# Kernel optimization log

Hardware: AMD Instinct MI355X
Metric: run time of the kernel (lower is better)

The kernel has to match this reference:

```python
import jax, jax.numpy as jnp
import numpy as np

B, S, K, H = 2, 2048, 32, 8
IN, DM, OUT = 768, 768, 768
HD = DM // H


def setup_inputs() -> dict:
    key = jax.random.key(0)
    k0, k1, k2, k3, k4 = jax.random.split(key, 5)
    x = jax.random.normal(k0, (B, S, IN), dtype=jnp.float32)
    neighbors = jax.random.randint(k1, (B, S, K), 0, S)  # base seq indices in [0, S)
    pad = jnp.arange(S) >= int(S * 0.95)
    mask = jnp.broadcast_to(pad[None, :, None], (B, S, 1))
    # MaskedLinear to_qkv: weight (3*DM, IN), bias (3*DM); to_out: (OUT, DM), no bias
    W_qkv = jax.random.normal(k2, (3 * DM, IN), dtype=jnp.float32) * (IN ** -0.5)
    b_qkv = jax.random.normal(k3, (3 * DM,), dtype=jnp.float32) * 0.01
    W_out = jax.random.normal(k4, (OUT, DM), dtype=jnp.float32) * (DM ** -0.5)
    return {"x": x, "W_qkv": W_qkv, "b_qkv": b_qkv, "W_out": W_out,
            "neighbors": neighbors, "mask": mask}


def reference(x, W_qkv, b_qkv, W_out, neighbors, mask):
    scale = HD ** -0.5
    # to_qkv (MaskedLinear, mask_value=0.0): padded rows zeroed after projection
    qkv = x @ W_qkv.T + b_qkv                      # (B, S, 3*DM)
    qkv = jnp.where(mask, 0.0, qkv)
    q, k, v = jnp.split(qkv, 3, axis=-1)
    split_heads = lambda t: t.reshape(B, S, H, HD).transpose(0, 2, 1, 3)  # (B,H,S,HD)
    q, k, v = split_heads(q), split_heads(k), split_heads(v)

    # gather K neighbors per query (same neighbor list across heads)
    bi = jnp.arange(B)[:, None, None, None]
    hi = jnp.arange(H)[None, :, None, None]
    nb = jnp.broadcast_to(neighbors[:, None, :, :], (B, H, S, K))
    k_nb = k[bi, hi, nb]                            # (B, H, S, K, HD)
    v_nb = v[bi, hi, nb]                            # (B, H, S, K, HD)

    attn = jnp.einsum('bhnd,bhnkd->bhnk', q, k_nb) * scale  # (B, H, S, K)
    # mask gathered at neighbor positions: padded neighbors get -inf
    m_nb = mask[:, :, 0][jnp.arange(B)[:, None, None], neighbors]  # (B, S, K)
    attn = jnp.where(m_nb[:, None, :, :], -jnp.inf, attn)
    w = jax.nn.softmax(attn, axis=-1)               # dropout = 0.0

    out = jnp.einsum('bhnk,bhnkd->bhnd', w, v_nb)   # (B, H, S, HD)
    out = out.transpose(0, 2, 1, 3).reshape(B, S, DM)
    # to_out (MaskedLinear, bias=False, mask_value=0.0)
    out = out @ W_out.T
    out = jnp.where(mask, 0.0, out)
    return out
```

## Files before the change

kernel.cpp:

```cpp
#include <hip/hip_runtime.h>
#include <hip/hip_bf16.h>
#include <math.h>


#define S_LEN 2048
#define NPAD 1945
#define DMODEL 768
#define LDAB 1536

typedef __attribute__((ext_vector_type(4))) float f32x4;
typedef __attribute__((ext_vector_type(8))) _Float16 f16x8;
typedef __attribute__((ext_vector_type(4))) _Float16 f16x4;

static __device__ __forceinline__ void async16(const void* g, void* l) {
  __builtin_amdgcn_global_load_lds(
      (const __attribute__((address_space(1))) unsigned int*)g,
      (__attribute__((address_space(3))) unsigned int*)l, 16, 0, 0);
}

__global__ __launch_bounds__(256) void cast3_kernel(
    const float* __restrict__ x, const float* __restrict__ wq,
    const float* __restrict__ wo,
    _Float16* __restrict__ Ah, _Float16* __restrict__ Bq,
    _Float16* __restrict__ Bo)
{
  int i = blockIdx.x * 256 + threadIdx.x;
  const float* s; _Float16* d; int off;
  if (i < 786432)       { s = x;  d = Ah; off = i; }
  else if (i < 1228800) { s = wq; d = Bq; off = i - 786432; }
  else if (i < 1376256) { s = wo; d = Bo; off = i - 1228800; }
  else return;
  float4 v = ((const float4*)s)[off];
  f16x4 o = {(_Float16)v.x, (_Float16)v.y, (_Float16)v.z, (_Float16)v.w};
  ((f16x4*)d)[off] = o;
}

template<int BN, bool QKV>
__global__ __launch_bounds__(256, 2) void gemm_f16(
    const _Float16* __restrict__ A,
    const _Float16* __restrict__ B,
    const float* __restrict__ bias,
    float* __restrict__ C,
    _Float16* __restrict__ Kh, _Float16* __restrict__ Vh,
    int N)
{
  constexpr int NF = BN / 32;
  constexpr int NISS = (128 + BN) / 64;
  __shared__ _Float16 As[2][128 * 32];
  __shared__ _Float16 Bs[2][BN * 32];
  const int t = threadIdx.x;
  const int lane = t & 63;
  const int wave = t >> 6;
  const int wr = wave >> 1, wc = wave & 1;
  const int lr = lane & 15, lg = lane >> 4;

  const int nwg_x = gridDim.x;
  const int nwg = nwg_x * gridDim.y;
  int bid = blockIdx.y * nwg_x + blockIdx.x;
  bid = (bid & 7) * (nwg >> 3) + (bid >> 3);
  const int brow = (bid % nwg_x) * 128;
  const int bcol = (bid / nwg_x) * BN;

  const char* gA = (const char*)A + (size_t)brow * LDAB;
  const char* gB = (const char*)B + (size_t)bcol * LDAB;

  auto stage = [&](int bb, int kt) {
    const int kb = kt * 64;
#pragma unroll
    for (int i = 0; i < NISS; ++i) {
      const int off = i * 4096 + t * 16;
      if (off < 8192) {
        async16(gA + (size_t)(off >> 6) * LDAB + kb + (off & 63),
                (char*)As[bb] + off);
      } else {
        const int oo = off - 8192;
        async16(gB + (size_t)(oo >> 6) * LDAB + kb + (oo & 63),
                (char*)Bs[bb] + oo);
      }
    }
  };

  f32x4 acc[4][NF];
#pragma unroll
  for (int i = 0; i < 4; ++i)
#pragma unroll
    for (int j = 0; j < NF; ++j) acc[i][j] = (f32x4)0.f;

  stage(0, 0);
  __syncthreads();

  int cur = 0;
  for (int kt = 0; kt < 24; ++kt) {
    if (kt + 1 < 24) stage(cur ^ 1, kt + 1);

    f16x8 af[4], bf[NF];
#pragma unroll
    for (int m = 0; m < 4; ++m)
      af[m] = *(const f16x8*)((const char*)As[cur] + (wr * 64 + m * 16 + lr) * 64 + lg * 16);
#pragma unroll
    for (int n = 0; n < NF; ++n)
      bf[n] = *(const f16x8*)((const char*)Bs[cur] + (wc * (BN / 2) + n * 16 + lr) * 64 + lg * 16);
#pragma unroll
    for (int m = 0; m < 4; ++m)
#pragma unroll
      for (int n = 0; n < NF; ++n)
        acc[m][n] = __builtin_amdgcn_mfma_f32_16x16x32_f16(af[m], bf[n],
                                                           acc[m][n], 0, 0, 0);
    __syncthreads();
    cur ^= 1;
  }

#pragma unroll
  for (int m = 0; m < 4; ++m) {
    const int row0 = brow + wr * 64 + m * 16 + lg * 4;
#pragma unroll
    for (int n = 0; n < NF; ++n) {
      const int col = bcol + wc * (BN / 2) + n * 16 + lr;
      const float bs = bias ? bias[col] : 0.f;
      f32x4 v = acc[m][n];
#pragma unroll
      for (int r = 0; r < 4; ++r) {
        const int rg = row0 + r;
        const int s = rg & (S_LEN - 1);
        const float val = (s >= NPAD) ? 0.f : (v[r] + bs);
        if (QKV) {
          if (col < DMODEL) {
            C[(size_t)rg * DMODEL + col] = val;
          } else if (col < 2 * DMODEL) {
            const int e = col - DMODEL;
            const int ch = e >> 3, o = e & 7;
            const int h = ch / 12, k = ch % 12;
            Kh[(size_t)rg * DMODEL + ((h + 8 * k) << 3) + o] = (_Float16)val;
          } else {
            Vh[(size_t)rg * DMODEL + (col - 2 * DMODEL)] = (_Float16)val;
          }
        } else {
          C[(size_t)rg * N + col] = val;
        }
      }
    }
  }
}

#define NPRE 12
__global__ __launch_bounds__(256) void attn_kernel(
    const float* __restrict__ Qf,
    const _Float16* __restrict__ Kh,
    const _Float16* __restrict__ Vh,
    const int* __restrict__ neighbors,
    _Float16* __restrict__ Ao)
{
  const int bid = blockIdx.x;
  const int xcd = bid & 7, slot = bid >> 3;
  const int bch = xcd >> 2;
  const int s   = slot * 4 + (xcd & 3);
  const int m   = bch * S_LEN + s;
  const int t   = threadIdx.x;

  _Float16* orow = Ao + (size_t)m * DMODEL;
  if (s >= NPAD) {
    if (t < 192) ((f16x4*)orow)[t] = (f16x4)(_Float16)0.f;
    return;
  }

  __shared__ float qs2[8 * 100];
  __shared__ float scf[288];
  __shared__ float ws[256];
  __shared__ int nb[32];

  if (t < 32) nb[t] = neighbors[(size_t)m * 32 + t];
  if (t < 192) {
    float4 v = ((const float4*)(Qf + (size_t)m * DMODEL))[t];
    const int h = t / 24, wi = t * 4 - h * 96;
    *(float4*)(qs2 + h * 100 + wi) = v;
  }
  __syncthreads();

  f16x4 vpre[NPRE];
  if (t < 192) {
#pragma unroll
    for (int jj = 0; jj < NPRE; ++jj)
      vpre[jj] = *(const f16x4*)(Vh + (size_t)(bch * S_LEN + nb[jj]) * DMODEL + t * 4);
  }

  {
    const int lane = t & 63, w = t >> 6;
    const int r = lane >> 3, h = lane & 7;
    const int j = w * 8 + r;
    const _Float16* kbase = Kh + (size_t)(bch * S_LEN + nb[j]) * DMODEL;
    f16x8 kv[12];
#pragma unroll
    for (int k = 0; k < 12; ++k)
      kv[k] = *(const f16x8*)(kbase + ((h + 8 * k) << 3));
    float sc = 0.f;
#pragma unroll
    for (int k = 0; k < 12; ++k) {
      const float4 qa = *(const float4*)(qs2 + h * 100 + k * 8);
      const float4 qb = *(const float4*)(qs2 + h * 100 + k * 8 + 4);
      sc += (float)kv[k][0] * qa.x + (float)kv[k][1] * qa.y +
            (float)kv[k][2] * qa.z + (float)kv[k][3] * qa.w +
            (float)kv[k][4] * qb.x + (float)kv[k][5] * qb.y +
            (float)kv[k][6] * qb.z + (float)kv[k][7] * qb.w;
    }
    scf[j * 9 + h] = sc * 0.10206207261596575f;
  }
  __syncthreads();

  {
    const int h = t >> 5, j = t & 31;
    const bool masked = (nb[j] >= NPAD);
    const float sc = scf[j * 9 + h];
    float mx = masked ? -1e30f : sc;
#pragma unroll
    for (int off = 16; off >= 1; off >>= 1) mx = fmaxf(mx, __shfl_xor(mx, off));
    float p = masked ? 0.f : expf(sc - mx);
    float sum = p;
#pragma unroll
    for (int off = 16; off >= 1; off >>= 1) sum += __shfl_xor(sum, off);
    ws[t] = p / sum;
  }
  __syncthreads();

  if (t < 192) {
    const int d0 = t * 4;
    const int hh = t / 24;
    const float* wsh = ws + hh * 32;
    f32x4 acc = (f32x4)0.f;
#pragma unroll
    for (int jj = 0; jj < NPRE; ++jj) {
      const float w = wsh[jj];
      acc[0] += w * (float)vpre[jj][0];
      acc[1] += w * (float)vpre[jj][1];
      acc[2] += w * (float)vpre[jj][2];
      acc[3] += w * (float)vpre[jj][3];
    }
#pragma unroll 8
    for (int jj = NPRE; jj < 32; ++jj) {
      const f16x4 v = *(const f16x4*)(Vh + (size_t)(bch * S_LEN + nb[jj]) * DMODEL + d0);
      const float w = wsh[jj];
      acc[0] += w * (float)v[0];
      acc[1] += w * (float)v[1];
      acc[2] += w * (float)v[2];
      acc[3] += w * (float)v[3];
    }
    f16x4 o = {(_Float16)acc[0], (_Float16)acc[1], (_Float16)acc[2], (_Float16)acc[3]};
    ((f16x4*)orow)[t] = o;
  }
}

extern "C" void kernel_launch(void* const* d_in, const int* in_sizes, int n_in,
                              void* d_out, int out_size, void* d_ws, size_t ws_size,
                              hipStream_t stream) {
  const float* x       = (const float*)d_in[0];
  const float* W_qkv   = (const float*)d_in[1];
  const float* b_qkv   = (const float*)d_in[2];
  const float* W_out   = (const float*)d_in[3];
  const int*   nbr     = (const int*)d_in[4];
  float* out = (float*)d_out;

  char* ws = (char*)d_ws;
  _Float16* Ah = (_Float16*)(ws);
  _Float16* Bq = (_Float16*)(ws +  6291456);
  _Float16* Bo = (_Float16*)(ws +  9830400);
  float*    Qf = (float*)   (ws + 11010048);
  _Float16* Kh = (_Float16*)(ws + 23592960);
  _Float16* Vh = (_Float16*)(ws + 29884416);
  _Float16* Ao = Ah;

  cast3_kernel<<<5376, 256, 0, stream>>>(x, W_qkv, W_out, Ah, Bq, Bo);

  gemm_f16<128, true><<<dim3(32, 18), 256, 0, stream>>>(Ah, Bq, b_qkv,
                                                        Qf, Kh, Vh, 3 * DMODEL);
  attn_kernel<<<4096, 256, 0, stream>>>(Qf, Kh, Vh, nbr, Ao);
  gemm_f16<64, false><<<dim3(32, 12), 256, 0, stream>>>(Ao, Bo, nullptr,
                                                        out, nullptr, nullptr, DMODEL);
}
```

Before: 156.1 us.

## Halve GEMM M-tile and process two query rows per attention block

The GEMMs now take a template BM and use 64-row tiles with launch bounds of 4 waves per SIMD, which doubles the grid so more workgroups fill the CUs. The attention kernel handles two consecutive queries per block, interleaving their K and V gathers to raise memory-level parallelism and halving the block count. It also drops the V prefetch into registers. Risks are more tile overhead and B reloads in the GEMMs, plus higher register pressure and a branch in the attention inner loop.

```diff
diff --git a/kernel.cpp b/kernel.cpp
--- a/kernel.cpp
+++ b/kernel.cpp
@@ -35,8 +35,8 @@
   ((f16x4*)d)[off] = o;
 }
 
-template<int BN, bool QKV>
-__global__ __launch_bounds__(256, 2) void gemm_f16(
+template<int BM, int BN, bool QKV>
+__global__ __launch_bounds__(256, 4) void gemm_f16(
     const _Float16* __restrict__ A,
     const _Float16* __restrict__ B,
     const float* __restrict__ bias,
@@ -44,9 +44,11 @@
     _Float16* __restrict__ Kh, _Float16* __restrict__ Vh,
     int N)
 {
+  constexpr int MF = BM / 32;
   constexpr int NF = BN / 32;
-  constexpr int NISS = (128 + BN) / 64;
-  __shared__ _Float16 As[2][128 * 32];
+  constexpr int ABYTES = BM * 64;
+  constexpr int NISS = (BM + BN) / 64;
+  __shared__ _Float16 As[2][BM * 32];
   __shared__ _Float16 Bs[2][BN * 32];
   const int t = threadIdx.x;
   const int lane = t & 63;
@@ -58,7 +60,7 @@
   const int nwg = nwg_x * gridDim.y;
   int bid = blockIdx.y * nwg_x + blockIdx.x;
   bid = (bid & 7) * (nwg >> 3) + (bid >> 3);
-  const int brow = (bid % nwg_x) * 128;
+  const int brow = (bid % nwg_x) * BM;
   const int bcol = (bid / nwg_x) * BN;
 
   const char* gA = (const char*)A + (size_t)brow * LDAB;
@@ -69,20 +71,20 @@
 #pragma unroll
     for (int i = 0; i < NISS; ++i) {
       const int off = i * 4096 + t * 16;
-      if (off < 8192) {
+      if (off < ABYTES) {
         async16(gA + (size_t)(off >> 6) * LDAB + kb + (off & 63),
                 (char*)As[bb] + off);
       } else {
-        const int oo = off - 8192;
+        const int oo = off - ABYTES;
         async16(gB + (size_t)(oo >> 6) * LDAB + kb + (oo & 63),
                 (char*)Bs[bb] + oo);
       }
     }
   };
 
-  f32x4 acc[4][NF];
-#pragma unroll
-  for (int i = 0; i < 4; ++i)
+  f32x4 acc[MF][NF];
+#pragma unroll
+  for (int i = 0; i < MF; ++i)
 #pragma unroll
     for (int j = 0; j < NF; ++j) acc[i][j] = (f32x4)0.f;
 
@@ -93,15 +95,15 @@
   for (int kt = 0; kt < 24; ++kt) {
     if (kt + 1 < 24) stage(cur ^ 1, kt + 1);
 
-    f16x8 af[4], bf[NF];
-#pragma unroll
-    for (int m = 0; m < 4; ++m)
-      af[m] = *(const f16x8*)((const char*)As[cur] + (wr * 64 + m * 16 + lr) * 64 + lg * 16);
+    f16x8 af[MF], bf[NF];
+#pragma unroll
+    for (int m = 0; m < MF; ++m)
+      af[m] = *(const f16x8*)((const char*)As[cur] + (wr * (BM / 2) + m * 16 + lr) * 64 + lg * 16);
 #pragma unroll
     for (int n = 0; n < NF; ++n)
       bf[n] = *(const f16x8*)((const char*)Bs[cur] + (wc * (BN / 2) + n * 16 + lr) * 64 + lg * 16);
 #pragma unroll
-    for (int m = 0; m < 4; ++m)
+    for (int m = 0; m < MF; ++m)
 #pragma unroll
       for (int n = 0; n < NF; ++n)
         acc[m][n] = __builtin_amdgcn_mfma_f32_16x16x32_f16(af[m], bf[n],
@@ -111,8 +113,8 @@
   }
 
 #pragma unroll
-  for (int m = 0; m < 4; ++m) {
-    const int row0 = brow + wr * 64 + m * 16 + lg * 4;
+  for (int m = 0; m < MF; ++m) {
+    const int row0 = brow + wr * (BM / 2) + m * 16 + lg * 4;
 #pragma unroll
     for (int n = 0; n < NF; ++n) {
       const int col = bcol + wc * (BN / 2) + n * 16 + lr;
@@ -142,7 +144,6 @@
   }
 }
 
-#define NPRE 12
 __global__ __launch_bounds__(256) void attn_kernel(
     const float* __restrict__ Qf,
     const _Float16* __restrict__ Kh,
@@ -153,98 +154,132 @@
   const int bid = blockIdx.x;
   const int xcd = bid & 7, slot = bid >> 3;
   const int bch = xcd >> 2;
-  const int s   = slot * 4 + (xcd & 3);
-  const int m   = bch * S_LEN + s;
+  const int u   = slot * 4 + (xcd & 3);
+  const int s0  = u * 2, s1 = s0 + 1;
+  const int m0  = bch * S_LEN + s0, m1 = m0 + 1;
   const int t   = threadIdx.x;
 
-  _Float16* orow = Ao + (size_t)m * DMODEL;
-  if (s >= NPAD) {
-    if (t < 192) ((f16x4*)orow)[t] = (f16x4)(_Float16)0.f;
+  _Float16* orow0 = Ao + (size_t)m0 * DMODEL;
+  _Float16* orow1 = Ao + (size_t)m1 * DMODEL;
+  const bool act0 = (s0 < NPAD), act1 = (s1 < NPAD);
+  if (!act0) {
+    if (t < 192) {
+      ((f16x4*)orow0)[t] = (f16x4)(_Float16)0.f;
+      ((f16x4*)orow1)[t] = (f16x4)(_Float16)0.f;
+    }
     return;
   }
 
-  __shared__ float qs2[8 * 100];
-  __shared__ float scf[288];
-  __shared__ float ws[256];
-  __shared__ int nb[32];
-
-  if (t < 32) nb[t] = neighbors[(size_t)m * 32 + t];
-  if (t < 192) {
-    float4 v = ((const float4*)(Qf + (size_t)m * DMODEL))[t];
-    const int h = t / 24, wi = t * 4 - h * 96;
-    *(float4*)(qs2 + h * 100 + wi) = v;
+  __shared__ float qs2[2][800];
+  __shared__ float scf[2][288];
+  __shared__ float ws[2][256];
+  __shared__ int nb[2][32];
+
+  if (t < 64) nb[t >> 5][t & 31] = neighbors[(size_t)m0 * 32 + t];
+  {
+    if (t < 192) {
+      float4 v = ((const float4*)(Qf + (size_t)m0 * DMODEL))[t];
+      const int h = t / 24, wi = t * 4 - h * 96;
+      *(float4*)(qs2[0] + h * 100 + wi) = v;
+    }
+    if (t >= 64) {
+      const int i = t - 64;
+      float4 v = ((const float4*)(Qf + (size_t)m1 * DMODEL))[i];
+      const int h = i / 24, wi = i * 4 - h * 96;
+      *(float4*)(qs2[1] + h * 100 + wi) = v;
+    }
   }
   __syncthreads();
-
-  f16x4 vpre[NPRE];
-  if (t < 192) {
-#pragma unroll
-    for (int jj = 0; jj < NPRE; ++jj)
-      vpre[jj] = *(const f16x4*)(Vh + (size_t)(bch * S_LEN + nb[jj]) * DMODEL + t * 4);
-  }
 
   {
     const int lane = t & 63, w = t >> 6;
-    const int r = lane >> 3, h = lane & 7;
-    const int j = w * 8 + r;
-    const _Float16* kbase = Kh + (size_t)(bch * S_LEN + nb[j]) * DMODEL;
-    f16x8 kv[12];
-#pragma unroll
-    for (int k = 0; k < 12; ++k)
-      kv[k] = *(const f16x8*)(kbase + ((h + 8 * k) << 3));
-    float sc = 0.f;
+    const int nbw = lane >> 3, h = lane & 7;
+    const int j = w * 8 + nbw;
+    const _Float16* kb0 = Kh + (size_t)(bch * S_LEN + nb[0][j]) * DMODEL;
+    const _Float16* kb1 = Kh + (size_t)(bch * S_LEN + nb[1][j]) * DMODEL;
+    float sc0 = 0.f, sc1 = 0.f;
 #pragma unroll
     for (int k = 0; k < 12; ++k) {
-      const float4 qa = *(const float4*)(qs2 + h * 100 + k * 8);
-      const float4 qb = *(const float4*)(qs2 + h * 100 + k * 8 + 4);
-      sc += (float)kv[k][0] * qa.x + (float)kv[k][1] * qa.y +
-            (float)kv[k][2] * qa.z + (float)kv[k][3] * qa.w +
-            (float)kv[k][4] * qb.x + (float)kv[k][5] * qb.y +
-            (float)kv[k][6] * qb.z + (float)kv[k][7] * qb.w;
-    }
-    scf[j * 9 + h] = sc * 0.10206207261596575f;
+      const f16x8 k0 = *(const f16x8*)(kb0 + ((h + 8 * k) << 3));
+      const f16x8 k1 = *(const f16x8*)(kb1 + ((h + 8 * k) << 3));
+      const float4 qa0 = *(const float4*)(qs2[0] + h * 100 + k * 8);
+      const float4 qb0 = *(const float4*)(qs2[0] + h * 100 + k * 8 + 4);
+      const float4 qa1 = *(const float4*)(qs2[1] + h * 100 + k * 8);
+      const float4 qb1 = *(const float4*)(qs2[1] + h * 100 + k * 8 + 4);
+      sc0 += (float)k0[0] * qa0.x + (float)k0[1] * qa0.y +
+             (float)k0[2] * qa0.z + (float)k0[3] * qa0.w +
+             (float)k0[4] * qb0.x + (float)k0[5] * qb0.y +
+             (float)k0[6] * qb0.z + (float)k0[7] * qb0.w;
+      sc1 += (float)k1[0] * qa1.x + (float)k1[1] * qa1.y +
+             (float)k1[2] * qa1.z + (float)k1[3] * qa1.w +
+             (float)k1[4] * qb1.x + (float)k1[5] * qb1.y +
+             (float)k1[6] * qb1.z + (float)k1[7] * qb1.w;
+    }
+    scf[0][j * 9 + h] = sc0 * 0.10206207261596575f;
+    scf[1][j * 9 + h] = sc1 * 0.10206207261596575f;
   }
   __syncthreads();
 
   {
     const int h = t >> 5, j = t & 31;
-    const bool masked = (nb[j] >= NPAD);
-    const float sc = scf[j * 9 + h];
-    float mx = masked ? -1e30f : sc;
-#pragma unroll
-    for (int off = 16; off >= 1; off >>= 1) mx = fmaxf(mx, __shfl_xor(mx, off));
-    float p = masked ? 0.f : expf(sc - mx);
-    float sum = p;
-#pragma unroll
-    for (int off = 16; off >= 1; off >>= 1) sum += __shfl_xor(sum, off);
-    ws[t] = p / sum;
+    {
+      const bool masked = (nb[0][j] >= NPAD);
+      const float sc = scf[0][j * 9 + h];
+      float mx = masked ? -1e30f : sc;
+#pragma unroll
+      for (int off = 16; off >= 1; off >>= 1) mx = fmaxf(mx, __shfl_xor(mx, off));
+      float p = masked ? 0.f : expf(sc - mx);
+      float sum = p;
+#pragma unroll
+      for (int off = 16; off >= 1; off >>= 1) sum += __shfl_xor(sum, off);
+      ws[0][t] = p / sum;
+    }
+    if (act1) {
+      const bool masked = (nb[1][j] >= NPAD);
+      const float sc = scf[1][j * 9 + h];
+      float mx = masked ? -1e30f : sc;
+#pragma unroll
+      for (int off = 16; off >= 1; off >>= 1) mx = fmaxf(mx, __shfl_xor(mx, off));
+      float p = masked ? 0.f : expf(sc - mx);
+      float sum = p;
+#pragma unroll
+      for (int off = 16; off >= 1; off >>= 1) sum += __shfl_xor(sum, off);
+      ws[1][t] = p / sum;
+    }
   }
   __syncthreads();
 
   if (t < 192) {
     const int d0 = t * 4;
     const int hh = t / 24;
-    const float* wsh = ws + hh * 32;
-    f32x4 acc = (f32x4)0.f;
-#pragma unroll
-    for (int jj = 0; jj < NPRE; ++jj) {
-      const float w = wsh[jj];
-      acc[0] += w * (float)vpre[jj][0];
-      acc[1] += w * (float)vpre[jj][1];
-      acc[2] += w * (float)vpre[jj][2];
-      acc[3] += w * (float)vpre[jj][3];
-    }
+    const float* wsh0 = ws[0] + hh * 32;
+    const float* wsh1 = ws[1] + hh * 32;
+    f32x4 acc0 = (f32x4)0.f, acc1 = (f32x4)0.f;
 #pragma unroll 8
-    for (int jj = NPRE; jj < 32; ++jj) {
-      const f16x4 v = *(const f16x4*)(Vh + (size_t)(bch * S_LEN + nb[jj]) * DMODEL + d0);
-      const float w = wsh[jj];
-      acc[0] += w * (float)v[0];
-      acc[1] += w * (float)v[1];
-      acc[2] += w * (float)v[2];
-      acc[3] += w * (float)v[3];
-    }
-    f16x4 o = {(_Float16)acc[0], (_Float16)acc[1], (_Float16)acc[2], (_Float16)acc[3]};
-    ((f16x4*)orow)[t] = o;
+    for (int jj = 0; jj < 32; ++jj) {
+      const f16x4 v0 = *(const f16x4*)(Vh + (size_t)(bch * S_LEN + nb[0][jj]) * DMODEL + d0);
+      const float w0 = wsh0[jj];
+      acc0[0] += w0 * (float)v0[0];
+      acc0[1] += w0 * (float)v0[1];
+      acc0[2] += w0 * (float)v0[2];
+      acc0[3] += w0 * (float)v0[3];
+      if (act1) {
+        const f16x4 v1 = *(const f16x4*)(Vh + (size_t)(bch * S_LEN + nb[1][jj]) * DMODEL + d0);
+        const float w1 = wsh1[jj];
+        acc1[0] += w1 * (float)v1[0];
+        acc1[1] += w1 * (float)v1[1];
+        acc1[2] += w1 * (float)v1[2];
+        acc1[3] += w1 * (float)v1[3];
+      }
+    }
+    f16x4 o0 = {(_Float16)acc0[0], (_Float16)acc0[1], (_Float16)acc0[2], (_Float16)acc0[3]};
+    ((f16x4*)orow0)[t] = o0;
+    if (act1) {
+      f16x4 o1 = {(_Float16)acc1[0], (_Float16)acc1[1], (_Float16)acc1[2], (_Float16)acc1[3]};
+      ((f16x4*)orow1)[t] = o1;
+    } else {
+      ((f16x4*)orow1)[t] = (f16x4)(_Float16)0.f;
+    }
   }
 }
 
@@ -269,9 +304,9 @@
 
   cast3_kernel<<<5376, 256, 0, stream>>>(x, W_qkv, W_out, Ah, Bq, Bo);
 
-  gemm_f16<128, true><<<dim3(32, 18), 256, 0, stream>>>(Ah, Bq, b_qkv,
-                                                        Qf, Kh, Vh, 3 * DMODEL);
-  attn_kernel<<<4096, 256, 0, stream>>>(Qf, Kh, Vh, nbr, Ao);
-  gemm_f16<64, false><<<dim3(32, 12), 256, 0, stream>>>(Ao, Bo, nullptr,
-                                                        out, nullptr, nullptr, DMODEL);
-}
+  gemm_f16<64, 128, true><<<dim3(64, 18), 256, 0, stream>>>(Ah, Bq, b_qkv,
+                                                            Qf, Kh, Vh, 3 * DMODEL);
+  attn_kernel<<<2048, 256, 0, stream>>>(Qf, Kh, Vh, nbr, Ao);
+  gemm_f16<64, 64, false><<<dim3(64, 12), 256, 0, stream>>>(Ao, Bo, nullptr,
+                                                            out, nullptr, nullptr, DMODEL);
+}
```

Result: no change. 155.7 us (-0.3%).

## Split attention blocks by head-half over two queries and shrink GEMM M tiles

Applied to the files above, without the earlier changes.

The attention kernel now has each block handle two consecutive query rows for half of the heads (four heads, 384 dims), instead of one row for all eight heads. It also drops the V prefetch registers and loads K fragments inside the dot-product loop. Both GEMMs move from 128-row to 64-row tiles with twice as many workgroups and a launch bound of 4 blocks per SM, to fill more CUs. The cost is less data reuse per GEMM tile and possibly more exposed gather latency in attention, since the prefetch is gone.

```diff
diff --git a/kernel.cpp b/kernel.cpp
--- a/kernel.cpp
+++ b/kernel.cpp
@@ -35,8 +35,8 @@
   ((f16x4*)d)[off] = o;
 }
 
-template<int BN, bool QKV>
-__global__ __launch_bounds__(256, 2) void gemm_f16(
+template<int BM, int BN, bool QKV>
+__global__ __launch_bounds__(256, 4) void gemm_f16(
     const _Float16* __restrict__ A,
     const _Float16* __restrict__ B,
     const float* __restrict__ bias,
@@ -44,9 +44,11 @@
     _Float16* __restrict__ Kh, _Float16* __restrict__ Vh,
     int N)
 {
+  constexpr int MF = BM / 32;
   constexpr int NF = BN / 32;
-  constexpr int NISS = (128 + BN) / 64;
-  __shared__ _Float16 As[2][128 * 32];
+  constexpr int ABYTES = BM * 64;
+  constexpr int NISS = (BM + BN) / 64;
+  __shared__ _Float16 As[2][BM * 32];
   __shared__ _Float16 Bs[2][BN * 32];
   const int t = threadIdx.x;
   const int lane = t & 63;
@@ -58,7 +60,7 @@
   const int nwg = nwg_x * gridDim.y;
   int bid = blockIdx.y * nwg_x + blockIdx.x;
   bid = (bid & 7) * (nwg >> 3) + (bid >> 3);
-  const int brow = (bid % nwg_x) * 128;
+  const int brow = (bid % nwg_x) * BM;
   const int bcol = (bid / nwg_x) * BN;
 
   const char* gA = (const char*)A + (size_t)brow * LDAB;
@@ -69,20 +71,20 @@
 #pragma unroll
     for (int i = 0; i < NISS; ++i) {
       const int off = i * 4096 + t * 16;
-      if (off < 8192) {
+      if (off < ABYTES) {
         async16(gA + (size_t)(off >> 6) * LDAB + kb + (off & 63),
                 (char*)As[bb] + off);
       } else {
-        const int oo = off - 8192;
+        const int oo = off - ABYTES;
         async16(gB + (size_t)(oo >> 6) * LDAB + kb + (oo & 63),
                 (char*)Bs[bb] + oo);
       }
     }
   };
 
-  f32x4 acc[4][NF];
-#pragma unroll
-  for (int i = 0; i < 4; ++i)
+  f32x4 acc[MF][NF];
+#pragma unroll
+  for (int i = 0; i < MF; ++i)
 #pragma unroll
     for (int j = 0; j < NF; ++j) acc[i][j] = (f32x4)0.f;
 
@@ -93,15 +95,15 @@
   for (int kt = 0; kt < 24; ++kt) {
     if (kt + 1 < 24) stage(cur ^ 1, kt + 1);
 
-    f16x8 af[4], bf[NF];
-#pragma unroll
-    for (int m = 0; m < 4; ++m)
-      af[m] = *(const f16x8*)((const char*)As[cur] + (wr * 64 + m * 16 + lr) * 64 + lg * 16);
+    f16x8 af[MF], bf[NF];
+#pragma unroll
+    for (int m = 0; m < MF; ++m)
+      af[m] = *(const f16x8*)((const char*)As[cur] + (wr * (BM / 2) + m * 16 + lr) * 64 + lg * 16);
 #pragma unroll
     for (int n = 0; n < NF; ++n)
       bf[n] = *(const f16x8*)((const char*)Bs[cur] + (wc * (BN / 2) + n * 16 + lr) * 64 + lg * 16);
 #pragma unroll
-    for (int m = 0; m < 4; ++m)
+    for (int m = 0; m < MF; ++m)
 #pragma unroll
       for (int n = 0; n < NF; ++n)
         acc[m][n] = __builtin_amdgcn_mfma_f32_16x16x32_f16(af[m], bf[n],
@@ -111,8 +113,8 @@
   }
 
 #pragma unroll
-  for (int m = 0; m < 4; ++m) {
-    const int row0 = brow + wr * 64 + m * 16 + lg * 4;
+  for (int m = 0; m < MF; ++m) {
+    const int row0 = brow + wr * (BM / 2) + m * 16 + lg * 4;
 #pragma unroll
     for (int n = 0; n < NF; ++n) {
       const int col = bcol + wc * (BN / 2) + n * 16 + lr;
@@ -142,7 +144,6 @@
   }
 }
 
-#define NPRE 12
 __global__ __launch_bounds__(256) void attn_kernel(
     const float* __restrict__ Qf,
     const _Float16* __restrict__ Kh,
@@ -152,99 +153,97 @@
 {
   const int bid = blockIdx.x;
   const int xcd = bid & 7, slot = bid >> 3;
-  const int bch = xcd >> 2;
-  const int s   = slot * 4 + (xcd & 3);
-  const int m   = bch * S_LEN + s;
+  const int p   = xcd >> 1;
+  const int bch = p >> 1;
+  const int dh  = p & 1;
+  const int u   = slot * 2 + (xcd & 1);
+  const int s0  = u * 2, s1 = s0 + 1;
+  const int m0  = bch * S_LEN + s0, m1 = m0 + 1;
+  const int hbase = dh * 4, dbase = dh * 384;
   const int t   = threadIdx.x;
 
-  _Float16* orow = Ao + (size_t)m * DMODEL;
-  if (s >= NPAD) {
-    if (t < 192) ((f16x4*)orow)[t] = (f16x4)(_Float16)0.f;
+  _Float16* o0 = Ao + (size_t)m0 * DMODEL + dbase;
+  _Float16* o1 = Ao + (size_t)m1 * DMODEL + dbase;
+  const bool act1 = (s1 < NPAD);
+  if (s0 >= NPAD) {
+    if (t < 192) {
+      const int row = t / 96, i = t - row * 96;
+      ((f16x4*)(row ? o1 : o0))[i] = (f16x4)(_Float16)0.f;
+    }
     return;
   }
 
-  __shared__ float qs2[8 * 100];
-  __shared__ float scf[288];
-  __shared__ float ws[256];
-  __shared__ int nb[32];
-
-  if (t < 32) nb[t] = neighbors[(size_t)m * 32 + t];
+  __shared__ float qs[2][400];
+  __shared__ float scf[2][300];
+  __shared__ float ws[2][128];
+  __shared__ int nb[2][32];
+
+  if (t < 64) nb[t >> 5][t & 31] = neighbors[(size_t)m0 * 32 + t];
   if (t < 192) {
-    float4 v = ((const float4*)(Qf + (size_t)m * DMODEL))[t];
-    const int h = t / 24, wi = t * 4 - h * 96;
-    *(float4*)(qs2 + h * 100 + wi) = v;
-  }
-  __syncthreads();
-
-  f16x4 vpre[NPRE];
+    const int row = t / 96, i = t - row * 96;
+    float4 v = ((const float4*)(Qf + (size_t)(row ? m1 : m0) * DMODEL + dbase))[i];
+    const int h = i / 24, wi = (i - h * 24) * 4;
+    *(float4*)(qs[row] + h * 100 + wi) = v;
+  }
+  __syncthreads();
+
+  {
+    const int row = t >> 7, rem = t & 127;
+    const int h = rem & 3, j = rem >> 2;
+    const _Float16* kb = Kh + (size_t)(bch * S_LEN + nb[row][j]) * DMODEL;
+    float sc = 0.f;
+#pragma unroll
+    for (int k = 0; k < 12; ++k) {
+      const f16x8 kv = *(const f16x8*)(kb + ((hbase + h + 8 * k) << 3));
+      const float4 qa = *(const float4*)(qs[row] + h * 100 + k * 8);
+      const float4 qb = *(const float4*)(qs[row] + h * 100 + k * 8 + 4);
+      sc += (float)kv[0] * qa.x + (float)kv[1] * qa.y +
+            (float)kv[2] * qa.z + (float)kv[3] * qa.w +
+            (float)kv[4] * qb.x + (float)kv[5] * qb.y +
+            (float)kv[6] * qb.z + (float)kv[7] * qb.w;
+    }
+    scf[row][j * 9 + h] = sc * 0.10206207261596575f;
+  }
+  __syncthreads();
+
+  {
+    const int row = t >> 7, h = (t >> 5) & 3, j = t & 31;
+    const bool masked = (nb[row][j] >= NPAD);
+    const float sc = scf[row][j * 9 + h];
+    float mx = masked ? -1e30f : sc;
+#pragma unroll
+    for (int off = 16; off >= 1; off >>= 1) mx = fmaxf(mx, __shfl_xor(mx, off));
+    float pp = masked ? 0.f : expf(sc - mx);
+    float sum = pp;
+#pragma unroll
+    for (int off = 16; off >= 1; off >>= 1) sum += __shfl_xor(sum, off);
+    ws[row][h * 32 + j] = pp / sum;
+  }
+  __syncthreads();
+
   if (t < 192) {
-#pragma unroll
-    for (int jj = 0; jj < NPRE; ++jj)
-      vpre[jj] = *(const f16x4*)(Vh + (size_t)(bch * S_LEN + nb[jj]) * DMODEL + t * 4);
-  }
-
-  {
-    const int lane = t & 63, w = t >> 6;
-    const int r = lane >> 3, h = lane & 7;
-    const int j = w * 8 + r;
-    const _Float16* kbase = Kh + (size_t)(bch * S_LEN + nb[j]) * DMODEL;
-    f16x8 kv[12];
-#pragma unroll
-    for (int k = 0; k < 12; ++k)
-      kv[k] = *(const f16x8*)(kbase + ((h + 8 * k) << 3));
-    float sc = 0.f;
-#pragma unroll
-    for (int k = 0; k < 12; ++k) {
-      const float4 qa = *(const float4*)(qs2 + h * 100 + k * 8);
-      const float4 qb = *(const float4*)(qs2 + h * 100 + k * 8 + 4);
-      sc += (float)kv[k][0] * qa.x + (float)kv[k][1] * qa.y +
-            (float)kv[k][2] * qa.z + (float)kv[k][3] * qa.w +
-            (float)kv[k][4] * qb.x + (float)kv[k][5] * qb.y +
-            (float)kv[k][6] * qb.z + (float)kv[k][7] * qb.w;
-    }
-    scf[j * 9 + h] = sc * 0.10206207261596575f;
-  }
-  __syncthreads();
-
-  {
-    const int h = t >> 5, j = t & 31;
-    const bool masked = (nb[j] >= NPAD);
-    const float sc = scf[j * 9 + h];
-    float mx = masked ? -1e30f : sc;
-#pragma unroll
-    for (int off = 16; off >= 1; off >>= 1) mx = fmaxf(mx, __shfl_xor(mx, off));
-    float p = masked ? 0.f : expf(sc - mx);
-    float sum = p;
-#pragma unroll
-    for (int off = 16; off >= 1; off >>= 1) sum += __shfl_xor(sum, off);
-    ws[t] = p / sum;
-  }
-  __syncthreads();
-
-  if (t < 192) {
-    const int d0 = t * 4;
-    const int hh = t / 24;
-    const float* wsh = ws + hh * 32;
+    const int row = t / 96, i = t - row * 96;
+    const int d0 = dbase + i * 4;
+    const int h = i / 24;
+    const float* wsh = ws[row] + h * 32;
+    const int* nbr_ = nb[row];
     f32x4 acc = (f32x4)0.f;
-#pragma unroll
-    for (int jj = 0; jj < NPRE; ++jj) {
-      const float w = wsh[jj];
-      acc[0] += w * (float)vpre[jj][0];
-      acc[1] += w * (float)vpre[jj][1];
-      acc[2] += w * (float)vpre[jj][2];
-      acc[3] += w * (float)vpre[jj][3];
-    }
 #pragma unroll 8
-    for (int jj = NPRE; jj < 32; ++jj) {
-      const f16x4 v = *(const f16x4*)(Vh + (size_t)(bch * S_LEN + nb[jj]) * DMODEL + d0);
+    for (int jj = 0; jj < 32; ++jj) {
+      const f16x4 v = *(const f16x4*)(Vh + (size_t)(bch * S_LEN + nbr_[jj]) * DMODEL + d0);
       const float w = wsh[jj];
       acc[0] += w * (float)v[0];
       acc[1] += w * (float)v[1];
       acc[2] += w * (float)v[2];
       acc[3] += w * (float)v[3];
     }
-    f16x4 o = {(_Float16)acc[0], (_Float16)acc[1], (_Float16)acc[2], (_Float16)acc[3]};
-    ((f16x4*)orow)[t] = o;
+    _Float16* orow = row ? o1 : o0;
+    if (row == 1 && !act1) {
+      ((f16x4*)orow)[i] = (f16x4)(_Float16)0.f;
+    } else {
+      f16x4 o = {(_Float16)acc[0], (_Float16)acc[1], (_Float16)acc[2], (_Float16)acc[3]};
+      ((f16x4*)orow)[i] = o;
+    }
   }
 }
 
@@ -269,9 +268,9 @@
 
   cast3_kernel<<<5376, 256, 0, stream>>>(x, W_qkv, W_out, Ah, Bq, Bo);
 
-  gemm_f16<128, true><<<dim3(32, 18), 256, 0, stream>>>(Ah, Bq, b_qkv,
-                                                        Qf, Kh, Vh, 3 * DMODEL);
+  gemm_f16<64, 128, true><<<dim3(64, 18), 256, 0, stream>>>(Ah, Bq, b_qkv,
+                                                            Qf, Kh, Vh, 3 * DMODEL);
   attn_kernel<<<4096, 256, 0, stream>>>(Qf, Kh, Vh, nbr, Ao);
-  gemm_f16<64, false><<<dim3(32, 12), 256, 0, stream>>>(Ao, Bo, nullptr,
-                                                        out, nullptr, nullptr, DMODEL);
-}
+  gemm_f16<64, 64, false><<<dim3(64, 12), 256, 0, stream>>>(Ao, Bo, nullptr,
+                                                            out, nullptr, nullptr, DMODEL);
+}
```

New measurement: 160.3 us. 1.03x slower.
